# Kernel optimization log

Hardware: AMD Instinct MI355X
Metric: run time of the kernel (lower is better)

The kernel has to match this reference:

```python
import jax, jax.numpy as jnp
import numpy as np

N_NODES = 100000
EPS = 1e-12  # F.normalize eps


def mean_aggregate(x, src, dst):
    # gather source features along edges, segment-mean into destinations
    msg = x[src]                                              # [E, D]
    summed = jax.ops.segment_sum(msg, dst, num_segments=N_NODES)  # [N, D]
    cnt = jax.ops.segment_sum(jnp.ones_like(dst, dtype=x.dtype), dst,
                              num_segments=N_NODES)           # [N]
    return summed / jnp.maximum(cnt, 1.0)[:, None]


def sage_conv(x, src, dst, W_l, b_l, W_r, normalize):
    agg = mean_aggregate(x, src, dst)
    out = agg @ W_l.T + b_l + x @ W_r.T  # lin_l(mean neigh) + lin_r(root)
    if normalize:
        norm = jnp.sqrt(jnp.sum(out * out, axis=-1, keepdims=True))
        out = out / jnp.maximum(norm, EPS)
    return out


def setup_inputs() -> dict:
    key = jax.random.key(0)
    ks = jax.random.split(key, 8)
    H, O = 128, 128
    s = 1.0 / np.sqrt(H)
    x = jax.random.normal(ks[0], (N_NODES, H), dtype=jnp.float32)
    edge_index = jax.random.randint(ks[1], (2, 1600000), 0, N_NODES, dtype=jnp.int64)
    return {
        "x": x,
        "edge_index": edge_index,
        "W1l": jax.random.uniform(ks[2], (H, H), jnp.float32, -s, s),
        "b1": jax.random.uniform(ks[3], (H,), jnp.float32, -s, s),
        "W1r": jax.random.uniform(ks[4], (H, H), jnp.float32, -s, s),
        "W2l": jax.random.uniform(ks[5], (O, H), jnp.float32, -s, s),
        "b2": jax.random.uniform(ks[6], (O,), jnp.float32, -s, s),
        "W2r": jax.random.uniform(ks[7], (O, H), jnp.float32, -s, s),
    }


def reference(x, edge_index, W1l, b1, W1r, W2l, b2, W2r):
    src, dst = edge_index[0], edge_index[1]
    h = sage_conv(x, src, dst, W1l, b1, W1r, normalize=True)
    h = jax.nn.relu(h)
    out = sage_conv(h, src, dst, W2l, b2, W2r, normalize=False)
    return out
```

## Files before the change

kernel.cpp:

```cpp
#include <hip/hip_runtime.h>
#include <hip/hip_bf16.h>
#include <hip/hip_fp16.h>

#define N_NODES 100000
#define DFEAT 128
#define SLAB 4096
#define BSHIFT 9
#define NBUCK 196

#define WS_CNT      0
#define WS_GH       100000
#define WS_PARTB    180000
#define WS_OFFS     200000
#define WS_ESRC     300608
#define WS_AGGH     1900608
#define WS_CASTH    8300608

typedef _Float16 half8 __attribute__((ext_vector_type(8)));
typedef _Float16 half2v __attribute__((ext_vector_type(2)));
typedef float floatx4 __attribute__((ext_vector_type(4)));

__global__ __launch_bounds__(256) void prep_kernel(const float* __restrict__ x,
                                                   __half* __restrict__ xh, int total4,
                                                   const int* __restrict__ dst,
                                                   int* __restrict__ gh,
                                                   int E, int bpart, int castblocks) {
    __shared__ int lh[NBUCK];
    int b = blockIdx.x;
    if (b < castblocks) {
        int i = b * 256 + threadIdx.x;
        if (i < total4) {
            float4 v = ((const float4*)x)[i];
            __half2 h01 = __floats2half2_rn(v.x, v.y);
            __half2 h23 = __floats2half2_rn(v.z, v.w);
            uint2 o;
            o.x = *(unsigned int*)&h01;
            o.y = *(unsigned int*)&h23;
            ((uint2*)xh)[i] = o;
        }
        return;
    }
    int bb = b - castblocks;
    for (int i = threadIdx.x; i < NBUCK; i += 256) lh[i] = 0;
    __syncthreads();
    int s0 = bb * SLAB, s1 = min(E, s0 + SLAB);
    for (int i = s0 + threadIdx.x; i < s1; i += 256)
        atomicAdd(&lh[dst[i] >> BSHIFT], 1);
    __syncthreads();
    for (int i = threadIdx.x; i < NBUCK; i += 256) gh[i * bpart + bb] = lh[i];
}

__global__ void scan1_kernel(int* __restrict__ gh, int* __restrict__ partial, int m) {
    __shared__ int s[256];
    int i = blockIdx.x * 256 + threadIdx.x;
    int v = (i < m) ? gh[i] : 0;
    s[threadIdx.x] = v;
    __syncthreads();
    for (int d = 1; d < 256; d <<= 1) {
        int t = (threadIdx.x >= d) ? s[threadIdx.x - d] : 0;
        __syncthreads();
        s[threadIdx.x] += t;
        __syncthreads();
    }
    int incl = s[threadIdx.x];
    if (i < m) gh[i] = incl - v;
    if (threadIdx.x == 255) partial[blockIdx.x] = incl;
}

__global__ void scan2_kernel(int* __restrict__ partial, int nb) {
    __shared__ int s[512];
    int t = threadIdx.x;
    int v = (t < nb) ? partial[t] : 0;
    s[t] = v;
    __syncthreads();
    for (int d = 1; d < 512; d <<= 1) {
        int u = (t >= d) ? s[t - d] : 0;
        __syncthreads();
        s[t] += u;
        __syncthreads();
    }
    if (t < nb) partial[t] = s[t] - v;
}

__global__ void scan3_kernel(int* __restrict__ gh, const int* __restrict__ partial, int m) {
    int i = blockIdx.x * 256 + threadIdx.x;
    if (i < m) gh[i] += partial[blockIdx.x];
}

__global__ __launch_bounds__(256) void phase2_kernel(const int* __restrict__ src,
                                                     const int* __restrict__ dst,
                                                     const int* __restrict__ gbase,
                                                     int2* __restrict__ pairs,
                                                     int E, int bpart) {
    __shared__ int lbase[NBUCK];
    __shared__ int lcur[NBUCK];
    __shared__ int lgb[NBUCK];
    __shared__ int sc[256];
    __shared__ int2 lp[SLAB];
    int b = blockIdx.x;
    int t = threadIdx.x;
    for (int i = t; i < NBUCK; i += 256) lbase[i] = 0;
    __syncthreads();
    int s0 = b * SLAB, s1 = min(E, s0 + SLAB);
    for (int i = s0 + t; i < s1; i += 256)
        atomicAdd(&lbase[dst[i] >> BSHIFT], 1);
    __syncthreads();
    int v = (t < NBUCK) ? lbase[t] : 0;
    sc[t] = v;
    __syncthreads();
    for (int d = 1; d < 256; d <<= 1) {
        int u = (t >= d) ? sc[t - d] : 0;
        __syncthreads();
        sc[t] += u;
        __syncthreads();
    }
    if (t < NBUCK) {
        int excl = sc[t] - v;
        lbase[t] = excl;
        lcur[t] = excl;
        lgb[t] = gbase[t * bpart + b];
    }
    __syncthreads();
    for (int i = s0 + t; i < s1; i += 256) {
        int d = dst[i];
        int s = src[i];
        int bk = d >> BSHIFT;
        int pos = atomicAdd(&lcur[bk], 1);
        lp[pos] = make_int2(s, d);
    }
    __syncthreads();
    int m = s1 - s0;
    for (int i = t; i < m; i += 256) {
        int2 p = lp[i];
        int bk = p.y >> BSHIFT;
        pairs[lgb[bk] + (i - lbase[bk])] = p;
    }
}

__global__ __launch_bounds__(512) void phase3_kernel(const int2* __restrict__ pairs,
                                                     const int* __restrict__ gbase,
                                                     int* __restrict__ cnt,
                                                     int* __restrict__ offs,
                                                     int* __restrict__ esrc,
                                                     int E, int bpart, int n) {
    __shared__ int lcnt[512];
    __shared__ int sc[512];
    __shared__ int lexcl[512];
    int g = blockIdx.x;
    int node0 = g << BSHIFT;
    int t = threadIdx.x;
    lcnt[t] = 0;
    __syncthreads();
    int S = gbase[g * bpart];
    int Eg = (g == NBUCK - 1) ? E : gbase[(g + 1) * bpart];
    for (int i = S + t; i < Eg; i += 512)
        atomicAdd(&lcnt[pairs[i].y - node0], 1);
    __syncthreads();
    int v = lcnt[t];
    sc[t] = v;
    __syncthreads();
    for (int d = 1; d < 512; d <<= 1) {
        int u = (t >= d) ? sc[t - d] : 0;
        __syncthreads();
        sc[t] += u;
        __syncthreads();
    }
    int excl = sc[t] - v;
    lexcl[t] = excl;
    int nd = node0 + t;
    if (nd < n) {
        cnt[nd] = v;
        offs[nd] = S + excl;
    }
    __syncthreads();
    for (int i = S + t; i < Eg; i += 512) {
        int2 p = pairs[i];
        int pos = atomicAdd(&lexcl[p.y - node0], 1);
        esrc[S + pos] = p.x;
    }
}

__global__ void aggregate_kernel(const __half* __restrict__ feat, const int* __restrict__ esrc,
                                 const int* __restrict__ offs, const int* __restrict__ cnt,
                                 __half* __restrict__ agg, int n) {
    int wid = (blockIdx.x * blockDim.x + threadIdx.x) >> 6;
    int lane = threadIdx.x & 63;
    if (wid >= n) return;
    int beg = offs[wid];
    int deg = cnt[wid];
    int grp = lane >> 4;
    int colbase = (lane & 15) * 8;

    half2v s0 = (half2v)(_Float16)0;
    half2v s1 = (half2v)(_Float16)0;
    half2v s2 = (half2v)(_Float16)0;
    half2v s3 = (half2v)(_Float16)0;

    for (int base = 0; base < deg; base += 64) {
        int m = min(64, deg - base);
        int idx = (lane < m) ? esrc[beg + base + lane] : 0;
#pragma unroll 4
        for (int j = 0; j < m; j += 4) {
            int jj = j + grp;
            bool valid = jj < m;
            int sidx = __shfl(idx, valid ? jj : 0);
            uint4 raw = *(const uint4*)(feat + (size_t)sidx * DFEAT + colbase);
            if (!valid) { raw.x = 0u; raw.y = 0u; raw.z = 0u; raw.w = 0u; }
            s0 += *(half2v*)&raw.x;
            s1 += *(half2v*)&raw.y;
            s2 += *(half2v*)&raw.z;
            s3 += *(half2v*)&raw.w;
        }
    }
    float a[8];
    a[0] = (float)s0.x; a[1] = (float)s0.y;
    a[2] = (float)s1.x; a[3] = (float)s1.y;
    a[4] = (float)s2.x; a[5] = (float)s2.y;
    a[6] = (float)s3.x; a[7] = (float)s3.y;
#pragma unroll
    for (int k = 0; k < 8; k++) {
        a[k] += __shfl_xor(a[k], 16);
        a[k] += __shfl_xor(a[k], 32);
    }
    if (lane < 16) {
        float scale = 1.0f / fmaxf((float)deg, 1.0f);
        __half2 h0 = __floats2half2_rn(a[0] * scale, a[1] * scale);
        __half2 h1 = __floats2half2_rn(a[2] * scale, a[3] * scale);
        __half2 h2 = __floats2half2_rn(a[4] * scale, a[5] * scale);
        __half2 h3 = __floats2half2_rn(a[6] * scale, a[7] * scale);
        uint4 o;
        o.x = *(unsigned int*)&h0;
        o.y = *(unsigned int*)&h1;
        o.z = *(unsigned int*)&h2;
        o.w = *(unsigned int*)&h3;
        *(uint4*)(agg + (size_t)wid * DFEAT + colbase) = o;
    }
}

template <bool NORM_RELU>
__global__ __launch_bounds__(256) void gemm_mfma_kernel(
    const __half* __restrict__ A1_, const __half* __restrict__ A2_,
    const float* __restrict__ Wl, const float* __restrict__ Wr,
    const float* __restrict__ bias, float* __restrict__ out32,
    __half* __restrict__ out16, int n) {
    __shared__ __align__(16) _Float16 lw[128 * 136];

    const _Float16* A1 = (const _Float16*)A1_;
    const _Float16* A2 = (const _Float16*)A2_;

    const int lane = threadIdx.x & 63;
    const int w = threadIdx.x >> 6;
    const int quad = lane >> 4;
    const int l15 = lane & 15;
    const int i0 = blockIdx.x * 128 + w * 32;

    floatx4 acc[2][8];
#pragma unroll
    for (int nt = 0; nt < 2; nt++)
#pragma unroll
        for (int ft = 0; ft < 8; ft++)
            acc[nt][ft] = (floatx4){0.f, 0.f, 0.f, 0.f};

    int r0 = i0 + l15;      if (r0 >= n) r0 = n - 1;
    int r1 = i0 + 16 + l15; if (r1 >= n) r1 = n - 1;
    const int kq = quad * 8;

    for (int half = 0; half < 2; half++) {
        const float* __restrict__ W = half ? Wr : Wl;
        const _Float16* __restrict__ A = half ? A2 : A1;
        if (half) __syncthreads();
        {
            int t = threadIdx.x;
            int row = t >> 1;
            int cb = (t & 1) * 64;
            const float4* sp = (const float4*)(W + row * DFEAT + cb);
            unsigned int* dp = (unsigned int*)&lw[row * 136 + cb];
#pragma unroll
            for (int q = 0; q < 16; q++) {
                float4 v = sp[q];
                __half2 h01 = __floats2half2_rn(v.x, v.y);
                __half2 h23 = __floats2half2_rn(v.z, v.w);
                dp[q * 2] = *(unsigned int*)&h01;
                dp[q * 2 + 1] = *(unsigned int*)&h23;
            }
        }
        __syncthreads();
#pragma unroll
        for (int kc = 0; kc < DFEAT; kc += 32) {
            half8 b0 = *(const half8*)(A + (size_t)r0 * DFEAT + kc + kq);
            half8 b1 = *(const half8*)(A + (size_t)r1 * DFEAT + kc + kq);
#pragma unroll
            for (int ft = 0; ft < 8; ft++) {
                half8 a = *(const half8*)&lw[(ft * 16 + l15) * 136 + kc + kq];
                acc[0][ft] = __builtin_amdgcn_mfma_f32_16x16x32_f16(a, b0, acc[0][ft], 0, 0, 0);
                acc[1][ft] = __builtin_amdgcn_mfma_f32_16x16x32_f16(a, b1, acc[1][ft], 0, 0, 0);
            }
        }
    }

#pragma unroll
    for (int nt = 0; nt < 2; nt++) {
        int node = i0 + nt * 16 + l15;
        float v[8][4];
#pragma unroll
        for (int ft = 0; ft < 8; ft++) {
            const float4 bq = *(const float4*)(bias + ft * 16 + quad * 4);
            v[ft][0] = acc[nt][ft][0] + bq.x;
            v[ft][1] = acc[nt][ft][1] + bq.y;
            v[ft][2] = acc[nt][ft][2] + bq.z;
            v[ft][3] = acc[nt][ft][3] + bq.w;
        }
        if (NORM_RELU) {
            float ss = 0.f;
#pragma unroll
            for (int ft = 0; ft < 8; ft++)
#pragma unroll
                for (int r = 0; r < 4; r++) ss = fmaf(v[ft][r], v[ft][r], ss);
            ss += __shfl_xor(ss, 16);
            ss += __shfl_xor(ss, 32);
            float inv = 1.0f / fmaxf(sqrtf(ss), 1e-12f);
#pragma unroll
            for (int ft = 0; ft < 8; ft++)
#pragma unroll
                for (int r = 0; r < 4; r++) v[ft][r] = fmaxf(v[ft][r] * inv, 0.0f);
        }
        if (node < n) {
            if (NORM_RELU) {
                __half* op = (__half*)out16 + (size_t)node * DFEAT + quad * 4;
#pragma unroll
                for (int ft = 0; ft < 8; ft++) {
                    __half2 h01 = __floats2half2_rn(v[ft][0], v[ft][1]);
                    __half2 h23 = __floats2half2_rn(v[ft][2], v[ft][3]);
                    uint2 o;
                    o.x = *(unsigned int*)&h01;
                    o.y = *(unsigned int*)&h23;
                    *(uint2*)(op + ft * 16) = o;
                }
            } else {
                float* op = out32 + (size_t)node * DFEAT + quad * 4;
#pragma unroll
                for (int ft = 0; ft < 8; ft++)
                    *(float4*)(op + ft * 16) = make_float4(v[ft][0], v[ft][1], v[ft][2], v[ft][3]);
            }
        }
    }
}

extern "C" void kernel_launch(void* const* d_in, const int* in_sizes, int n_in,
                              void* d_out, int out_size, void* d_ws, size_t ws_size,
                              hipStream_t stream) {
    const float* x = (const float*)d_in[0];
    const int* edge_index = (const int*)d_in[1];
    const float* W1l = (const float*)d_in[2];
    const float* b1 = (const float*)d_in[3];
    const float* W1r = (const float*)d_in[4];
    const float* W2l = (const float*)d_in[5];
    const float* b2 = (const float*)d_in[6];
    const float* W2r = (const float*)d_in[7];
    float* out = (float*)d_out;

    const int E = in_sizes[1] / 2;
    const int n = in_sizes[0] / DFEAT;

    int* ws = (int*)d_ws;
    int* cnt = ws + WS_CNT;
    int* gh = ws + WS_GH;
    int* partialB = ws + WS_PARTB;
    int* offs = ws + WS_OFFS;
    int* esrc = ws + WS_ESRC;
    int2* pairs = (int2*)(ws + WS_AGGH);
    __half* aggh = (__half*)(ws + WS_AGGH);
    __half* casth = (__half*)(ws + WS_CASTH);

    const int* src = edge_index;
    const int* dst = edge_index + E;

    const int bpart = (E + SLAB - 1) / SLAB;
    const int m = NBUCK * bpart;
    const int blocksB = (m + 255) / 256;
    const int total4 = n * DFEAT / 4;
    const int castblocks = (total4 + 255) / 256;

    prep_kernel<<<castblocks + bpart, 256, 0, stream>>>(x, casth, total4, dst, gh,
                                                        E, bpart, castblocks);
    scan1_kernel<<<blocksB, 256, 0, stream>>>(gh, partialB, m);
    scan2_kernel<<<1, 512, 0, stream>>>(partialB, blocksB);
    scan3_kernel<<<blocksB, 256, 0, stream>>>(gh, partialB, m);

    phase2_kernel<<<bpart, 256, 0, stream>>>(src, dst, gh, pairs, E, bpart);
    phase3_kernel<<<NBUCK, 512, 0, stream>>>(pairs, gh, cnt, offs, esrc, E, bpart, n);

    const int aggb = (n * 64 + 255) / 256;
    const int gemmb = (n + 127) / 128;

    aggregate_kernel<<<aggb, 256, 0, stream>>>(casth, esrc, offs, cnt, aggh, n);
    gemm_mfma_kernel<true><<<gemmb, 256, 0, stream>>>(aggh, casth, W1l, W1r, b1, nullptr, aggh, n);

    aggregate_kernel<<<aggb, 256, 0, stream>>>(aggh, esrc, offs, cnt, casth, n);
    gemm_mfma_kernel<false><<<gemmb, 256, 0, stream>>>(casth, aggh, W2l, W2r, b2, out, nullptr, n);
}
```

Measured before the change: 354.1 us.

## Map one 16-lane group per node in aggregation with unrolled independent gathers

```diff
diff --git a/kernel.cpp b/kernel.cpp
--- a/kernel.cpp
+++ b/kernel.cpp
@@ -180,61 +180,85 @@
     }
 }
 
+#define ACC(c, r)                        \
+    s[c][0] += *(half2v*)&(r).x;         \
+    s[c][1] += *(half2v*)&(r).y;         \
+    s[c][2] += *(half2v*)&(r).z;         \
+    s[c][3] += *(half2v*)&(r).w;
+
 __global__ void aggregate_kernel(const __half* __restrict__ feat, const int* __restrict__ esrc,
                                  const int* __restrict__ offs, const int* __restrict__ cnt,
                                  __half* __restrict__ agg, int n) {
     int wid = (blockIdx.x * blockDim.x + threadIdx.x) >> 6;
     int lane = threadIdx.x & 63;
-    if (wid >= n) return;
-    int beg = offs[wid];
-    int deg = cnt[wid];
     int grp = lane >> 4;
-    int colbase = (lane & 15) * 8;
-
-    half2v s0 = (half2v)(_Float16)0;
-    half2v s1 = (half2v)(_Float16)0;
-    half2v s2 = (half2v)(_Float16)0;
-    half2v s3 = (half2v)(_Float16)0;
-
-    for (int base = 0; base < deg; base += 64) {
-        int m = min(64, deg - base);
-        int idx = (lane < m) ? esrc[beg + base + lane] : 0;
-#pragma unroll 4
-        for (int j = 0; j < m; j += 4) {
-            int jj = j + grp;
-            bool valid = jj < m;
-            int sidx = __shfl(idx, valid ? jj : 0);
-            uint4 raw = *(const uint4*)(feat + (size_t)sidx * DFEAT + colbase);
-            if (!valid) { raw.x = 0u; raw.y = 0u; raw.z = 0u; raw.w = 0u; }
-            s0 += *(half2v*)&raw.x;
-            s1 += *(half2v*)&raw.y;
-            s2 += *(half2v*)&raw.z;
-            s3 += *(half2v*)&raw.w;
-        }
-    }
+    int l15 = lane & 15;
+    int node = wid * 4 + grp;
+    if (node >= n) return;
+    int beg = offs[node];
+    int deg = cnt[node];
+    const _Float16* fbase = (const _Float16*)feat + l15 * 8;
+    const int* ep = esrc + beg;
+
+    half2v s[4][4];
+#pragma unroll
+    for (int c = 0; c < 4; c++)
+#pragma unroll
+        for (int k = 0; k < 4; k++) s[c][k] = (half2v)(_Float16)0;
+
+    int j = 0;
+    for (; j + 8 <= deg; j += 8) {
+        int i0 = ep[j + 0], i1 = ep[j + 1], i2 = ep[j + 2], i3 = ep[j + 3];
+        int i4 = ep[j + 4], i5 = ep[j + 5], i6 = ep[j + 6], i7 = ep[j + 7];
+        uint4 r0 = *(const uint4*)(fbase + (size_t)i0 * DFEAT);
+        uint4 r1 = *(const uint4*)(fbase + (size_t)i1 * DFEAT);
+        uint4 r2 = *(const uint4*)(fbase + (size_t)i2 * DFEAT);
+        uint4 r3 = *(const uint4*)(fbase + (size_t)i3 * DFEAT);
+        uint4 r4 = *(const uint4*)(fbase + (size_t)i4 * DFEAT);
+        uint4 r5 = *(const uint4*)(fbase + (size_t)i5 * DFEAT);
+        uint4 r6 = *(const uint4*)(fbase + (size_t)i6 * DFEAT);
+        uint4 r7 = *(const uint4*)(fbase + (size_t)i7 * DFEAT);
+        ACC(0, r0) ACC(1, r1) ACC(2, r2) ACC(3, r3)
+        ACC(0, r4) ACC(1, r5) ACC(2, r6) ACC(3, r7)
+    }
+    for (; j + 4 <= deg; j += 4) {
+        int i0 = ep[j + 0], i1 = ep[j + 1], i2 = ep[j + 2], i3 = ep[j + 3];
+        uint4 r0 = *(const uint4*)(fbase + (size_t)i0 * DFEAT);
+        uint4 r1 = *(const uint4*)(fbase + (size_t)i1 * DFEAT);
+        uint4 r2 = *(const uint4*)(fbase + (size_t)i2 * DFEAT);
+        uint4 r3 = *(const uint4*)(fbase + (size_t)i3 * DFEAT);
+        ACC(0, r0) ACC(1, r1) ACC(2, r2) ACC(3, r3)
+    }
+    if (j < deg) {
+        int rem = deg - j;
+        int i0 = ep[j];
+        int i1 = ep[j + (rem > 1 ? 1 : 0)];
+        int i2 = ep[j + (rem > 2 ? 2 : 0)];
+        uint4 r0 = *(const uint4*)(fbase + (size_t)i0 * DFEAT);
+        uint4 r1 = *(const uint4*)(fbase + (size_t)i1 * DFEAT);
+        uint4 r2 = *(const uint4*)(fbase + (size_t)i2 * DFEAT);
+        if (rem < 2) { r1.x = 0u; r1.y = 0u; r1.z = 0u; r1.w = 0u; }
+        if (rem < 3) { r2.x = 0u; r2.y = 0u; r2.z = 0u; r2.w = 0u; }
+        ACC(0, r0) ACC(1, r1) ACC(2, r2)
+    }
+
+    float scale = 1.0f / fmaxf((float)deg, 1.0f);
     float a[8];
-    a[0] = (float)s0.x; a[1] = (float)s0.y;
-    a[2] = (float)s1.x; a[3] = (float)s1.y;
-    a[4] = (float)s2.x; a[5] = (float)s2.y;
-    a[6] = (float)s3.x; a[7] = (float)s3.y;
-#pragma unroll
-    for (int k = 0; k < 8; k++) {
-        a[k] += __shfl_xor(a[k], 16);
-        a[k] += __shfl_xor(a[k], 32);
-    }
-    if (lane < 16) {
-        float scale = 1.0f / fmaxf((float)deg, 1.0f);
-        __half2 h0 = __floats2half2_rn(a[0] * scale, a[1] * scale);
-        __half2 h1 = __floats2half2_rn(a[2] * scale, a[3] * scale);
-        __half2 h2 = __floats2half2_rn(a[4] * scale, a[5] * scale);
-        __half2 h3 = __floats2half2_rn(a[6] * scale, a[7] * scale);
-        uint4 o;
-        o.x = *(unsigned int*)&h0;
-        o.y = *(unsigned int*)&h1;
-        o.z = *(unsigned int*)&h2;
-        o.w = *(unsigned int*)&h3;
-        *(uint4*)(agg + (size_t)wid * DFEAT + colbase) = o;
-    }
+#pragma unroll
+    for (int k = 0; k < 4; k++) {
+        a[2 * k]     = ((float)s[0][k].x + (float)s[1][k].x) + ((float)s[2][k].x + (float)s[3][k].x);
+        a[2 * k + 1] = ((float)s[0][k].y + (float)s[1][k].y) + ((float)s[2][k].y + (float)s[3][k].y);
+    }
+    __half2 h0 = __floats2half2_rn(a[0] * scale, a[1] * scale);
+    __half2 h1 = __floats2half2_rn(a[2] * scale, a[3] * scale);
+    __half2 h2 = __floats2half2_rn(a[4] * scale, a[5] * scale);
+    __half2 h3 = __floats2half2_rn(a[6] * scale, a[7] * scale);
+    uint4 o;
+    o.x = *(unsigned int*)&h0;
+    o.y = *(unsigned int*)&h1;
+    o.z = *(unsigned int*)&h2;
+    o.w = *(unsigned int*)&h3;
+    *(uint4*)(agg + (size_t)node * DFEAT + l15 * 8) = o;
 }
 
 template <bool NORM_RELU>
@@ -390,7 +414,8 @@
     phase2_kernel<<<bpart, 256, 0, stream>>>(src, dst, gh, pairs, E, bpart);
     phase3_kernel<<<NBUCK, 512, 0, stream>>>(pairs, gh, cnt, offs, esrc, E, bpart, n);
 
-    const int aggb = (n * 64 + 255) / 256;
+    const int nwaves = (n + 3) / 4;
+    const int aggb = (nwaves * 64 + 255) / 256;
     const int gemmb = (n + 127) / 128;
 
     aggregate_kernel<<<aggb, 256, 0, stream>>>(casth, esrc, offs, cnt, aggh, n);
```

Result: faster. 346.2 us (-2.2%).
